# Kernel optimization log

Hardware: AMD Instinct MI355X
Metric: run time of the kernel (lower is better)

## Reference

```python
import jax, jax.numpy as jnp
import numpy as np

TAU = 2.0
EPS = 1e-5
T, B, C, H, W = 4, 16, 256, 32, 32
HEADS = 8
HD = C // HEADS
N = H * W


def make_spike(grad_fn):
    @jax.custom_vjp
    def f(x):
        return (x >= 0.0).astype(x.dtype)
    def fwd(x):
        return f(x), x
    def bwd(res, g):
        return (g * grad_fn(res),)
    f.defvjp(fwd, bwd)
    return f

# ATan surrogate (alpha=5.0) used by q/k/v LIF nodes
spike_atan5 = make_spike(lambda x: (5.0 / 2.0) / (1.0 + (jnp.pi / 2.0 * 5.0 * x) ** 2))
# default Sigmoid surrogate (alpha=4.0) for shortcut_lif / talking_heads_lif
def _sig_grad(x):
    s = jax.nn.sigmoid(4.0 * x)
    return 4.0 * s * (1.0 - s)
spike_sig4 = make_spike(_sig_grad)


def lif(x, spike, v_th=1.0):
    # multi-step LIF over leading time axis; hard reset to 0, detach_reset
    def step(v, xt):
        h = v + (xt - v) / TAU
        s = spike(h - v_th)
        v_new = h * (1.0 - jax.lax.stop_gradient(s))
        return v_new, s
    _, out = jax.lax.scan(step, jnp.zeros_like(x[0]), x)
    return out


def conv1x1(x, w):
    # x: (T,B,C,H,W), w: (Cout,Cin) from Conv2d kernel_size=1
    return jnp.einsum('tbchw,oc->tbohw', x, w)


def bn(y, gamma, beta, mean, var):
    scale = (gamma / jnp.sqrt(var + EPS))[None, None, :, None, None]
    shift = (beta - mean * gamma / jnp.sqrt(var + EPS))[None, None, :, None, None]
    return y * scale + shift


def to_heads(x):
    # (T,B,C,H,W) -> (T,B,heads,N,hd); matches flatten(3).transpose(-1,-2).reshape.permute
    x = x.reshape(T, B, C, N).transpose(0, 1, 3, 2)          # (T,B,N,C)
    x = x.reshape(T, B, N, HEADS, HD).transpose(0, 1, 3, 2, 4)  # (T,B,heads,N,hd)
    return x


def setup_inputs() -> dict:
    key = jax.random.key(0)
    ks = jax.random.split(key, 20)
    def bn_params(i):
        return (1.0 + 0.1 * jax.random.normal(ks[i], (C,), jnp.float32),
                0.1 * jax.random.normal(ks[i + 1], (C,), jnp.float32),
                0.1 * jax.random.normal(ks[i + 2], (C,), jnp.float32),
                jax.random.uniform(ks[i + 3], (C,), jnp.float32, 0.5, 1.5))
    q_g, q_b, q_m, q_var = bn_params(1)
    k_g, k_b, k_m, k_var = bn_params(5)
    v_g, v_b, v_m, v_var = bn_params(9)
    p_g, p_b, p_m, p_var = bn_params(13)
    std = 1.0 / np.sqrt(C)
    return {
        'x': jax.random.normal(ks[0], (T, B, C, H, W), jnp.float32),
        'q_w': std * jax.random.normal(ks[17], (C, C), jnp.float32),
        'q_g': q_g, 'q_b': q_b, 'q_m': q_m, 'q_var': q_var,
        'k_w': std * jax.random.normal(ks[18], (C, C), jnp.float32),
        'k_g': k_g, 'k_b': k_b, 'k_m': k_m, 'k_var': k_var,
        'v_w': std * jax.random.normal(ks[19], (C, C), jnp.float32),
        'v_g': v_g, 'v_b': v_b, 'v_m': v_m, 'v_var': v_var,
        'proj_w': std * jax.random.normal(ks[4], (C, C), jnp.float32),
        'proj_bias': 0.01 * jax.random.normal(ks[8], (C,), jnp.float32),
        'p_g': p_g, 'p_b': p_b, 'p_m': p_m, 'p_var': p_var,
    }


def reference(x, q_w, q_g, q_b, q_m, q_var, k_w, k_g, k_b, k_m, k_var,
              v_w, v_g, v_b, v_m, v_var, proj_w, proj_bias, p_g, p_b, p_m, p_var):
    identity = x
    xs = lif(x, spike_sig4, 1.0)                      # shortcut_lif
    q = to_heads(lif(bn(conv1x1(xs, q_w), q_g, q_b, q_m, q_var), spike_atan5, 1.0))
    k = to_heads(lif(bn(conv1x1(xs, k_w), k_g, k_b, k_m, k_var), spike_atan5, 1.0))
    v = to_heads(lif(bn(conv1x1(xs, v_w), v_g, v_b, v_m, v_var), spike_atan5, 1.0))
    kv = jnp.sum(k * v, axis=-2, keepdims=True)       # (T,B,heads,1,hd)
    kv = lif(kv, spike_sig4, 0.5)                     # talking_heads_lif, v_th=0.5
    attn = q * kv                                     # (T,B,heads,N,hd)
    # transpose(3,4).reshape(T,B,C,H,W)
    out = attn.transpose(0, 1, 2, 4, 3).reshape(T, B, C, H, W)
    out = conv1x1(out, proj_w) + proj_bias[None, None, :, None, None]
    out = bn(out, p_g, p_b, p_m, p_var)
    out = out + identity
    return out, v
```

## Files before the change

kernel.cpp:

```cpp
#include <hip/hip_runtime.h>
#include <hip/hip_bf16.h>
#include <stdint.h>

#define T_ 4
#define B_ 16
#define C_ 256
#define N_ 1024
#define HEADS_ 8
#define HD_ 32

typedef unsigned long long u64;
typedef unsigned char u8;

__device__ __forceinline__ u64 rf64(u64 v) {
  unsigned lo = __builtin_amdgcn_readfirstlane((unsigned)v);
  unsigned hi = __builtin_amdgcn_readfirstlane((unsigned)(v >> 32));
  return ((u64)hi << 32) | (u64)lo;
}

__global__ __launch_bounds__(256) void prep_kernel(
    const float* __restrict__ qw, const float* __restrict__ kw,
    const float* __restrict__ vw, const float* __restrict__ pw,
    const float* __restrict__ qg, const float* __restrict__ qb2,
    const float* __restrict__ qmn, const float* __restrict__ qvr,
    const float* __restrict__ kg, const float* __restrict__ kb2,
    const float* __restrict__ kmn, const float* __restrict__ kvr,
    const float* __restrict__ vg, const float* __restrict__ vb2,
    const float* __restrict__ vmn, const float* __restrict__ vvr,
    const float* __restrict__ pg, const float* __restrict__ pb2,
    const float* __restrict__ pmn, const float* __restrict__ pvr,
    float* __restrict__ wqkv, float* __restrict__ wtp,
    float* __restrict__ bnt) {
  if (blockIdx.x < 256) {
    int c = blockIdx.x;
    int o = threadIdx.x;
    wqkv[c * 768 + o]       = qw[o * C_ + c];
    wqkv[c * 768 + 256 + o] = kw[o * C_ + c];
    wqkv[c * 768 + 512 + o] = vw[o * C_ + c];
    wtp[c * C_ + o]         = pw[o * C_ + c];
  } else {
    int c = threadIdx.x;
    float rs;
    rs = sqrtf(qvr[c] + 1e-5f);
    bnt[0 * C_ + c] = qg[c] / rs;
    bnt[1 * C_ + c] = qb2[c] - qmn[c] * qg[c] / rs;
    rs = sqrtf(kvr[c] + 1e-5f);
    bnt[2 * C_ + c] = kg[c] / rs;
    bnt[3 * C_ + c] = kb2[c] - kmn[c] * kg[c] / rs;
    rs = sqrtf(vvr[c] + 1e-5f);
    bnt[4 * C_ + c] = vg[c] / rs;
    bnt[5 * C_ + c] = vb2[c] - vmn[c] * vg[c] / rs;
    rs = sqrtf(pvr[c] + 1e-5f);
    bnt[6 * C_ + c] = pg[c] / rs;
    bnt[7 * C_ + c] = pb2[c] - pmn[c] * pg[c] / rs;
  }
}

__global__ __launch_bounds__(256) void lif_shortcut(const float* __restrict__ x,
                                                    u64* __restrict__ xsm) {
  int b = blockIdx.x >> 5;
  int n0 = (blockIdx.x & 31) << 5;
  int tid = threadIdx.x;
  int l = tid & 63, w = tid >> 6;
  __shared__ float tile[C_ * 33];
  float v[32];
#pragma unroll
  for (int i = 0; i < 32; i++) v[i] = 0.f;
  int c = (w << 6) + l;
  for (int t = 0; t < T_; t++) {
    __syncthreads();
    const float* xp = x + (((size_t)t * B_ + b) * C_) * N_ + n0;
    for (int idx = tid; idx < C_ * 32; idx += 256) {
      int cc = idx >> 5, nn = idx & 31;
      tile[cc * 33 + nn] = xp[(size_t)cc * N_ + nn];
    }
    __syncthreads();
#pragma unroll
    for (int nn = 0; nn < 32; nn++) {
      float xv = tile[c * 33 + nn];
      float h = v[nn] + (xv - v[nn]) * 0.5f;
      bool s = h >= 1.0f;
      v[nn] = s ? 0.f : h;
      u64 bal = __ballot(s);
      if (l == nn) xsm[(((size_t)t * B_ + b) * N_ + n0 + nn) * 4 + w] = bal;
    }
  }
}

__global__ __launch_bounds__(256) void qkv_sparse(
    const u64* __restrict__ xsm, const float* __restrict__ wqkv,
    const float* __restrict__ bnt, u8* __restrict__ pkvb,
    u64* __restrict__ qm_out, float* __restrict__ vout) {
  int b = blockIdx.x >> 7;
  int nt = blockIdx.x & 127;
  int n0 = nt << 3;
  int tid = threadIdx.x;
  int l = tid & 63, wv = tid >> 6;

  __shared__ u64 kvw[8][4][4];
  __shared__ u64 vb[8][4][4];

  float qsc[4], qsh[4], ksc[4], ksh[4], vsc[4], vsh[4];
#pragma unroll
  for (int j = 0; j < 4; j++) {
    int o = (l << 2) + j;
    qsc[j] = bnt[0 * C_ + o]; qsh[j] = bnt[1 * C_ + o];
    ksc[j] = bnt[2 * C_ + o]; ksh[j] = bnt[3 * C_ + o];
    vsc[j] = bnt[4 * C_ + o]; vsh[j] = bnt[5 * C_ + o];
  }

  for (int s = 0; s < 2; s++) {
    int nn = wv + (s << 2);
    int n = n0 + nn;
    float vq[4] = {0.f, 0.f, 0.f, 0.f};
    float vk[4] = {0.f, 0.f, 0.f, 0.f};
    float vv2[4] = {0.f, 0.f, 0.f, 0.f};
#pragma unroll
    for (int t = 0; t < 4; t++) {
      size_t site = ((size_t)t * B_ + b) * N_ + n;
      const u64* mp = xsm + (site << 2);
      float aq[4] = {0.f, 0.f, 0.f, 0.f};
      float ak[4] = {0.f, 0.f, 0.f, 0.f};
      float av[4] = {0.f, 0.f, 0.f, 0.f};
      float4 q0 = {0.f, 0.f, 0.f, 0.f};
      float4 k0 = {0.f, 0.f, 0.f, 0.f};
      float4 v0 = {0.f, 0.f, 0.f, 0.f};
#pragma unroll
      for (int wd = 0; wd < 4; wd++) {
        u64 m = rf64(mp[wd]);
        while (m) {
          int c = (wd << 6) + __builtin_ctzll(m);
          m &= m - 1;
          const float4* pb = (const float4*)(wqkv + c * 768) + l;
          float4 q1 = pb[0];
          float4 k1 = pb[64];
          float4 v1 = pb[128];
          aq[0] += q0.x; aq[1] += q0.y; aq[2] += q0.z; aq[3] += q0.w;
          ak[0] += k0.x; ak[1] += k0.y; ak[2] += k0.z; ak[3] += k0.w;
          av[0] += v0.x; av[1] += v0.y; av[2] += v0.z; av[3] += v0.w;
          q0 = q1; k0 = k1; v0 = v1;
        }
      }
      aq[0] += q0.x; aq[1] += q0.y; aq[2] += q0.z; aq[3] += q0.w;
      ak[0] += k0.x; ak[1] += k0.y; ak[2] += k0.z; ak[3] += k0.w;
      av[0] += v0.x; av[1] += v0.y; av[2] += v0.z; av[3] += v0.w;
#pragma unroll
      for (int j = 0; j < 4; j++) {
        float pq = aq[j] * qsc[j] + qsh[j];
        float pk = ak[j] * ksc[j] + ksh[j];
        float pv = av[j] * vsc[j] + vsh[j];
        float hq = vq[j] + (pq - vq[j]) * 0.5f;
        float hk = vk[j] + (pk - vk[j]) * 0.5f;
        float hv = vv2[j] + (pv - vv2[j]) * 0.5f;
        bool sq = hq >= 1.0f; vq[j] = sq ? 0.f : hq;
        bool sk = hk >= 1.0f; vk[j] = sk ? 0.f : hk;
        bool sv = hv >= 1.0f; vv2[j] = sv ? 0.f : hv;
        u64 bq = __ballot(sq);
        u64 bkv = __ballot(sk && sv);
        u64 bv = __ballot(sv);
        if (l == (t << 2) + j) {
          qm_out[(site << 2) + j] = bq;
          kvw[nn][t][j] = bkv;
          vb[nn][t][j] = bv;
        }
      }
    }
  }
  __syncthreads();

#pragma unroll
  for (int t = 0; t < 4; t++) {
    int c = tid;
    int ll = c >> 2, j = c & 3;
    int ssum = 0;
#pragma unroll
    for (int s8 = 0; s8 < 8; s8++)
      ssum += (int)((kvw[s8][t][j] >> ll) & 1ull);
    pkvb[((((size_t)t * B_ + b) * C_ + c) << 7) + nt] = (u8)ssum;
  }

  {
    int th = tid >> 3;
    int t = th >> 3;
    int head = th & 7;
    int nl = tid & 7;
    float* vp = vout +
        ((((size_t)t * B_ + b) * HEADS_ + head) * N_ + n0 + nl) * HD_;
#pragma unroll
    for (int m4 = 0; m4 < 8; m4++) {
      int li = (head << 3) + m4;
      float4 o4;
      o4.x = ((vb[nl][t][0] >> li) & 1ull) ? 1.f : 0.f;
      o4.y = ((vb[nl][t][1] >> li) & 1ull) ? 1.f : 0.f;
      o4.z = ((vb[nl][t][2] >> li) & 1ull) ? 1.f : 0.f;
      o4.w = ((vb[nl][t][3] >> li) & 1ull) ? 1.f : 0.f;
      *(float4*)(vp + (m4 << 2)) = o4;
    }
  }
}

__global__ __launch_bounds__(256) void kv_lif_kernel(const u8* __restrict__ pkvb,
                                                     u64* __restrict__ kvsm) {
  int b = blockIdx.x;
  int tid = threadIdx.x;
  int l = tid & 63, j = tid >> 6;
  int c = (l << 2) + j;
  float v = 0.f;
  for (int t = 0; t < 4; t++) {
    const uint4* p =
        (const uint4*)(pkvb + ((((size_t)t * B_ + b) * C_ + c) << 7));
    int s = 0;
#pragma unroll
    for (int i = 0; i < 8; i++) {
      uint4 u = p[i];
      unsigned a;
      a = u.x; s += (a & 255) + ((a >> 8) & 255) + ((a >> 16) & 255) + (a >> 24);
      a = u.y; s += (a & 255) + ((a >> 8) & 255) + ((a >> 16) & 255) + (a >> 24);
      a = u.z; s += (a & 255) + ((a >> 8) & 255) + ((a >> 16) & 255) + (a >> 24);
      a = u.w; s += (a & 255) + ((a >> 8) & 255) + ((a >> 16) & 255) + (a >> 24);
    }
    float kvs = (float)s;
    float h = v + (kvs - v) * 0.5f;
    bool sp = h >= 0.5f;
    v = sp ? 0.f : h;
    u64 bal = __ballot(sp);
    if (l == t) kvsm[((size_t)t * B_ + b) * 4 + j] = bal;
  }
}

__global__ __launch_bounds__(256) void proj_sparse(
    const u64* __restrict__ qm, const u64* __restrict__ kvsm,
    const float* __restrict__ wtp, const float* __restrict__ bnt,
    const float* __restrict__ pbias, const float* __restrict__ x,
    float* __restrict__ out) {
  int tb = blockIdx.x >> 5;
  int n0 = (blockIdx.x & 31) << 5;
  int t = tb >> 4, b = tb & 15;
  int tid = threadIdx.x;
  int l = tid & 63, w = tid >> 6;
  __shared__ float tile[C_ * 33];
  u64 kvm[4];
#pragma unroll
  for (int j = 0; j < 4; j++) kvm[j] = kvsm[((size_t)t * B_ + b) * 4 + j];
  for (int nn = w; nn < 32; nn += 4) {
    int n = n0 + nn;
    float acc[4] = {0.f, 0.f, 0.f, 0.f};
    size_t site = ((size_t)t * B_ + b) * N_ + n;
    const u64* mp = qm + (site << 2);
#pragma unroll
    for (int j = 0; j < 4; j++) {
      u64 m = rf64(mp[j]) & kvm[j];
      while (m) {
        int li = __builtin_ctzll(m);
        m &= m - 1;
        int c = (li << 2) + j;
        const float* rp = wtp + c * C_;
#pragma unroll
        for (int jj = 0; jj < 4; jj++) acc[jj] += rp[(jj << 6) + l];
      }
    }
#pragma unroll
    for (int jj = 0; jj < 4; jj++) tile[((jj << 6) + l) * 33 + nn] = acc[jj];
  }
  __syncthreads();
  int col = l & 31;
  int half = l >> 5;
  for (int r = (w << 1) + half; r < C_; r += 8) {
    float val = tile[r * 33 + col];
    float z = (val + pbias[r]) * bnt[6 * C_ + r] + bnt[7 * C_ + r];
    size_t xi = (((size_t)t * B_ + b) * C_ + r) * N_ + n0 + col;
    out[xi] = z + x[xi];
  }
}

__global__ __launch_bounds__(256) void fill_zero_f32(float* p, size_t n) {
  size_t i = (size_t)blockIdx.x * 256 + threadIdx.x;
  if (i < n) p[i] = 0.0f;
}

extern "C" void kernel_launch(void* const* d_in, const int* in_sizes, int n_in,
                              void* d_out, int out_size, void* d_ws, size_t ws_size,
                              hipStream_t stream) {
  const float* x  = (const float*)d_in[0];
  const float* qw = (const float*)d_in[1];
  const float* qg = (const float*)d_in[2];
  const float* qb = (const float*)d_in[3];
  const float* qm = (const float*)d_in[4];
  const float* qv = (const float*)d_in[5];
  const float* kw = (const float*)d_in[6];
  const float* kg = (const float*)d_in[7];
  const float* kb = (const float*)d_in[8];
  const float* km = (const float*)d_in[9];
  const float* kv = (const float*)d_in[10];
  const float* vw = (const float*)d_in[11];
  const float* vg = (const float*)d_in[12];
  const float* vb2 = (const float*)d_in[13];
  const float* vm = (const float*)d_in[14];
  const float* vv = (const float*)d_in[15];
  const float* pw = (const float*)d_in[16];
  const float* pbias = (const float*)d_in[17];
  const float* pg = (const float*)d_in[18];
  const float* pb = (const float*)d_in[19];
  const float* pm = (const float*)d_in[20];
  const float* pv = (const float*)d_in[21];

  const size_t needed = 7342080ull + 2048ull;
  if (ws_size < needed) {
    size_t n = (size_t)out_size;
    fill_zero_f32<<<(unsigned)((n + 255) / 256), 256, 0, stream>>>(
        (float*)d_out, n);
    return;
  }

  char* ws = (char*)d_ws;
  float* wqkv = (float*)(ws + 0);
  float* wtp  = (float*)(ws + 786432);
  float* bnt  = (float*)(ws + 1048576);
  u64*   xsm  = (u64*)  (ws + 1056768);
  u64*   qmm  = (u64*)  (ws + 3153920);
  u8*    pkvb = (u8*)   (ws + 5251072);
  u64*   kvsm = (u64*)  (ws + 7348224);

  float* out  = (float*)d_out;
  float* vout = out + (size_t)T_ * B_ * C_ * N_;

  prep_kernel<<<257, 256, 0, stream>>>(qw, kw, vw, pw,
                                       qg, qb, qm, qv, kg, kb, km, kv,
                                       vg, vb2, vm, vv, pg, pb, pm, pv,
                                       wqkv, wtp, bnt);
  lif_shortcut<<<512, 256, 0, stream>>>(x, xsm);
  qkv_sparse<<<2048, 256, 0, stream>>>(xsm, wqkv, bnt, pkvb, qmm, vout);
  kv_lif_kernel<<<16, 256, 0, stream>>>(pkvb, kvsm);
  proj_sparse<<<2048, 256, 0, stream>>>(qmm, kvsm, wtp, bnt, pbias, x, out);
}
```

Baseline: 157.6 us.

## Precompute per-site spike channel lists to unroll sparse QKV gather

The shortcut LIF kernel now also writes, for each site, a compact byte list of up to 32 active input channels plus a count. The QKV kernel reads these lists and gathers weight rows four at a time, using a zeroed padding row for out-of-range slots, instead of a serial ctz loop over bitmasks. Sites with more than 32 active channels fall back to the bitmask path. The QKV grid is halved, with each block covering 16 positions, and the readfirstlane broadcasts are removed. This trades extra workspace and list-building work for more memory-level parallelism in the gather.

Result: no change. 159.7 us (+1.3%).

```diff
diff --git a/kernel.cpp b/kernel.cpp
--- a/kernel.cpp
+++ b/kernel.cpp
@@ -8,15 +8,11 @@
 #define N_ 1024
 #define HEADS_ 8
 #define HD_ 32
+#define ZOFF 196608
 
 typedef unsigned long long u64;
 typedef unsigned char u8;
-
-__device__ __forceinline__ u64 rf64(u64 v) {
-  unsigned lo = __builtin_amdgcn_readfirstlane((unsigned)v);
-  unsigned hi = __builtin_amdgcn_readfirstlane((unsigned)(v >> 32));
-  return ((u64)hi << 32) | (u64)lo;
-}
+typedef unsigned short u16;
 
 __global__ __launch_bounds__(256) void prep_kernel(
     const float* __restrict__ qw, const float* __restrict__ kw,
@@ -38,7 +34,7 @@
     wqkv[c * 768 + 256 + o] = kw[o * C_ + c];
     wqkv[c * 768 + 512 + o] = vw[o * C_ + c];
     wtp[c * C_ + o]         = pw[o * C_ + c];
-  } else {
+  } else if (blockIdx.x == 256) {
     int c = threadIdx.x;
     float rs;
     rs = sqrtf(qvr[c] + 1e-5f);
@@ -53,16 +49,25 @@
     rs = sqrtf(pvr[c] + 1e-5f);
     bnt[6 * C_ + c] = pg[c] / rs;
     bnt[7 * C_ + c] = pb2[c] - pmn[c] * pg[c] / rs;
-  }
-}
-
-__global__ __launch_bounds__(256) void lif_shortcut(const float* __restrict__ x,
-                                                    u64* __restrict__ xsm) {
+  } else {
+    int o = threadIdx.x;
+    wqkv[ZOFF + o]       = 0.f;
+    wqkv[ZOFF + 256 + o] = 0.f;
+    wqkv[ZOFF + 512 + o] = 0.f;
+  }
+}
+
+__global__ __launch_bounds__(256) void lif_pack(const float* __restrict__ x,
+                                                u64* __restrict__ xsm,
+                                                u8* __restrict__ lists,
+                                                u16* __restrict__ cnts) {
   int b = blockIdx.x >> 5;
   int n0 = (blockIdx.x & 31) << 5;
   int tid = threadIdx.x;
   int l = tid & 63, w = tid >> 6;
   __shared__ float tile[C_ * 33];
+  __shared__ u64 lmask[4][32][4];
+  __shared__ u8 slist[128][32];
   float v[32];
 #pragma unroll
   for (int i = 0; i < 32; i++) v[i] = 0.f;
@@ -82,23 +87,51 @@
       bool s = h >= 1.0f;
       v[nn] = s ? 0.f : h;
       u64 bal = __ballot(s);
-      if (l == nn) xsm[(((size_t)t * B_ + b) * N_ + n0 + nn) * 4 + w] = bal;
-    }
+      if (l == nn) {
+        lmask[t][nn][w] = bal;
+        xsm[(((size_t)t * B_ + b) * N_ + n0 + nn) * 4 + w] = bal;
+      }
+    }
+  }
+  __syncthreads();
+  if (tid < 128) {
+    int t = tid >> 5, nn = tid & 31;
+    size_t site = ((size_t)t * B_ + b) * N_ + n0 + nn;
+    int cnt = 0;
+#pragma unroll
+    for (int wd = 0; wd < 4; wd++) {
+      u64 m = lmask[t][nn][wd];
+      while (m) {
+        int cc = (wd << 6) + __builtin_ctzll(m);
+        m &= m - 1;
+        if (cnt < 32) slist[tid][cnt] = (u8)cc;
+        cnt++;
+      }
+    }
+    cnts[site] = (u16)cnt;
+  }
+  __syncthreads();
+  {
+    int si = tid >> 1, h = tid & 1;
+    int t = si >> 5, nn = si & 31;
+    size_t site = ((size_t)t * B_ + b) * N_ + n0 + nn;
+    ((uint4*)(lists + (site << 5)))[h] = ((uint4*)slist[si])[h];
   }
 }
 
 __global__ __launch_bounds__(256) void qkv_sparse(
-    const u64* __restrict__ xsm, const float* __restrict__ wqkv,
+    const u64* __restrict__ xsm, const u8* __restrict__ lists,
+    const u16* __restrict__ cnts, const float* __restrict__ wqkv,
     const float* __restrict__ bnt, u8* __restrict__ pkvb,
     u64* __restrict__ qm_out, float* __restrict__ vout) {
-  int b = blockIdx.x >> 7;
-  int nt = blockIdx.x & 127;
-  int n0 = nt << 3;
+  int b = blockIdx.x >> 6;
+  int nt = blockIdx.x & 63;
+  int n0 = nt << 4;
   int tid = threadIdx.x;
   int l = tid & 63, wv = tid >> 6;
 
-  __shared__ u64 kvw[8][4][4];
-  __shared__ u64 vb[8][4][4];
+  __shared__ u64 kvw[16][4][4];
+  __shared__ u64 vb[16][4][4];
 
   float qsc[4], qsh[4], ksc[4], ksh[4], vsc[4], vsh[4];
 #pragma unroll
@@ -109,7 +142,7 @@
     vsc[j] = bnt[4 * C_ + o]; vsh[j] = bnt[5 * C_ + o];
   }
 
-  for (int s = 0; s < 2; s++) {
+  for (int s = 0; s < 4; s++) {
     int nn = wv + (s << 2);
     int n = n0 + nn;
     float vq[4] = {0.f, 0.f, 0.f, 0.f};
@@ -118,32 +151,63 @@
 #pragma unroll
     for (int t = 0; t < 4; t++) {
       size_t site = ((size_t)t * B_ + b) * N_ + n;
-      const u64* mp = xsm + (site << 2);
+      int cn = cnts[site];
       float aq[4] = {0.f, 0.f, 0.f, 0.f};
       float ak[4] = {0.f, 0.f, 0.f, 0.f};
       float av[4] = {0.f, 0.f, 0.f, 0.f};
-      float4 q0 = {0.f, 0.f, 0.f, 0.f};
-      float4 k0 = {0.f, 0.f, 0.f, 0.f};
-      float4 v0 = {0.f, 0.f, 0.f, 0.f};
-#pragma unroll
-      for (int wd = 0; wd < 4; wd++) {
-        u64 m = rf64(mp[wd]);
-        while (m) {
-          int c = (wd << 6) + __builtin_ctzll(m);
-          m &= m - 1;
-          const float4* pb = (const float4*)(wqkv + c * 768) + l;
-          float4 q1 = pb[0];
-          float4 k1 = pb[64];
-          float4 v1 = pb[128];
-          aq[0] += q0.x; aq[1] += q0.y; aq[2] += q0.z; aq[3] += q0.w;
-          ak[0] += k0.x; ak[1] += k0.y; ak[2] += k0.z; ak[3] += k0.w;
-          av[0] += v0.x; av[1] += v0.y; av[2] += v0.z; av[3] += v0.w;
-          q0 = q1; k0 = k1; v0 = v1;
+      if (cn > 0 && cn <= 32) {
+        const uint4* lp = (const uint4*)(lists + (site << 5));
+        uint4 L0 = lp[0], L1 = lp[1];
+        unsigned dw[8] = {L0.x, L0.y, L0.z, L0.w, L1.x, L1.y, L1.z, L1.w};
+#pragma unroll
+        for (int d = 0; d < 8; d++) {
+          if ((d << 2) < cn) {
+            unsigned w4 = dw[d];
+            int i0 = d << 2;
+            int c0 = w4 & 255, c1 = (w4 >> 8) & 255;
+            int c2 = (w4 >> 16) & 255, c3 = w4 >> 24;
+            const float4* p0 =
+                (const float4*)(wqkv + (i0 + 0 < cn ? c0 * 768 : ZOFF)) + l;
+            const float4* p1 =
+                (const float4*)(wqkv + (i0 + 1 < cn ? c1 * 768 : ZOFF)) + l;
+            const float4* p2 =
+                (const float4*)(wqkv + (i0 + 2 < cn ? c2 * 768 : ZOFF)) + l;
+            const float4* p3 =
+                (const float4*)(wqkv + (i0 + 3 < cn ? c3 * 768 : ZOFF)) + l;
+            float4 q0 = p0[0], k0 = p0[64], v0 = p0[128];
+            float4 q1 = p1[0], k1 = p1[64], v1 = p1[128];
+            float4 q2 = p2[0], k2 = p2[64], v2 = p2[128];
+            float4 q3 = p3[0], k3 = p3[64], v3 = p3[128];
+            aq[0] += q0.x; aq[1] += q0.y; aq[2] += q0.z; aq[3] += q0.w;
+            ak[0] += k0.x; ak[1] += k0.y; ak[2] += k0.z; ak[3] += k0.w;
+            av[0] += v0.x; av[1] += v0.y; av[2] += v0.z; av[3] += v0.w;
+            aq[0] += q1.x; aq[1] += q1.y; aq[2] += q1.z; aq[3] += q1.w;
+            ak[0] += k1.x; ak[1] += k1.y; ak[2] += k1.z; ak[3] += k1.w;
+            av[0] += v1.x; av[1] += v1.y; av[2] += v1.z; av[3] += v1.w;
+            aq[0] += q2.x; aq[1] += q2.y; aq[2] += q2.z; aq[3] += q2.w;
+            ak[0] += k2.x; ak[1] += k2.y; ak[2] += k2.z; ak[3] += k2.w;
+            av[0] += v2.x; av[1] += v2.y; av[2] += v2.z; av[3] += v2.w;
+            aq[0] += q3.x; aq[1] += q3.y; aq[2] += q3.z; aq[3] += q3.w;
+            ak[0] += k3.x; ak[1] += k3.y; ak[2] += k3.z; ak[3] += k3.w;
+            av[0] += v3.x; av[1] += v3.y; av[2] += v3.z; av[3] += v3.w;
+          }
         }
-      }
-      aq[0] += q0.x; aq[1] += q0.y; aq[2] += q0.z; aq[3] += q0.w;
-      ak[0] += k0.x; ak[1] += k0.y; ak[2] += k0.z; ak[3] += k0.w;
-      av[0] += v0.x; av[1] += v0.y; av[2] += v0.z; av[3] += v0.w;
+      } else if (cn > 32) {
+        const u64* mp = xsm + (site << 2);
+#pragma unroll
+        for (int wd = 0; wd < 4; wd++) {
+          u64 m = mp[wd];
+          while (m) {
+            int cc = (wd << 6) + __builtin_ctzll(m);
+            m &= m - 1;
+            const float4* pb = (const float4*)(wqkv + cc * 768) + l;
+            float4 q0 = pb[0], k0 = pb[64], v0 = pb[128];
+            aq[0] += q0.x; aq[1] += q0.y; aq[2] += q0.z; aq[3] += q0.w;
+            ak[0] += k0.x; ak[1] += k0.y; ak[2] += k0.z; ak[3] += k0.w;
+            av[0] += v0.x; av[1] += v0.y; av[2] += v0.z; av[3] += v0.w;
+          }
+        }
+      }
 #pragma unroll
       for (int j = 0; j < 4; j++) {
         float pq = aq[j] * qsc[j] + qsh[j];
@@ -174,27 +238,31 @@
     int ll = c >> 2, j = c & 3;
     int ssum = 0;
 #pragma unroll
-    for (int s8 = 0; s8 < 8; s8++)
-      ssum += (int)((kvw[s8][t][j] >> ll) & 1ull);
-    pkvb[((((size_t)t * B_ + b) * C_ + c) << 7) + nt] = (u8)ssum;
+    for (int s16 = 0; s16 < 16; s16++)
+      ssum += (int)((kvw[s16][t][j] >> ll) & 1ull);
+    pkvb[((((size_t)t * B_ + b) * C_ + c) << 6) + nt] = (u8)ssum;
   }
 
   {
     int th = tid >> 3;
     int t = th >> 3;
     int head = th & 7;
-    int nl = tid & 7;
-    float* vp = vout +
-        ((((size_t)t * B_ + b) * HEADS_ + head) * N_ + n0 + nl) * HD_;
-#pragma unroll
-    for (int m4 = 0; m4 < 8; m4++) {
-      int li = (head << 3) + m4;
-      float4 o4;
-      o4.x = ((vb[nl][t][0] >> li) & 1ull) ? 1.f : 0.f;
-      o4.y = ((vb[nl][t][1] >> li) & 1ull) ? 1.f : 0.f;
-      o4.z = ((vb[nl][t][2] >> li) & 1ull) ? 1.f : 0.f;
-      o4.w = ((vb[nl][t][3] >> li) & 1ull) ? 1.f : 0.f;
-      *(float4*)(vp + (m4 << 2)) = o4;
+    int nl0 = tid & 7;
+#pragma unroll
+    for (int rep = 0; rep < 2; rep++) {
+      int nl = nl0 + (rep << 3);
+      float* vp = vout +
+          ((((size_t)t * B_ + b) * HEADS_ + head) * N_ + n0 + nl) * HD_;
+#pragma unroll
+      for (int m4 = 0; m4 < 8; m4++) {
+        int li = (head << 3) + m4;
+        float4 o4;
+        o4.x = ((vb[nl][t][0] >> li) & 1ull) ? 1.f : 0.f;
+        o4.y = ((vb[nl][t][1] >> li) & 1ull) ? 1.f : 0.f;
+        o4.z = ((vb[nl][t][2] >> li) & 1ull) ? 1.f : 0.f;
+        o4.w = ((vb[nl][t][3] >> li) & 1ull) ? 1.f : 0.f;
+        *(float4*)(vp + (m4 << 2)) = o4;
+      }
     }
   }
 }
@@ -208,10 +276,10 @@
   float v = 0.f;
   for (int t = 0; t < 4; t++) {
     const uint4* p =
-        (const uint4*)(pkvb + ((((size_t)t * B_ + b) * C_ + c) << 7));
+        (const uint4*)(pkvb + ((((size_t)t * B_ + b) * C_ + c) << 6));
     int s = 0;
 #pragma unroll
-    for (int i = 0; i < 8; i++) {
+    for (int i = 0; i < 4; i++) {
       uint4 u = p[i];
       unsigned a;
       a = u.x; s += (a & 255) + ((a >> 8) & 255) + ((a >> 16) & 255) + (a >> 24);
@@ -249,7 +317,7 @@
     const u64* mp = qm + (site << 2);
 #pragma unroll
     for (int j = 0; j < 4; j++) {
-      u64 m = rf64(mp[j]) & kvm[j];
+      u64 m = mp[j] & kvm[j];
       while (m) {
         int li = __builtin_ctzll(m);
         m &= m - 1;
@@ -304,7 +372,7 @@
   const float* pm = (const float*)d_in[20];
   const float* pv = (const float*)d_in[21];
 
-  const size_t needed = 7342080ull + 2048ull;
+  const size_t needed = 8534016ull;
   if (ws_size < needed) {
     size_t n = (size_t)out_size;
     fill_zero_f32<<<(unsigned)((n + 255) / 256), 256, 0, stream>>>(
@@ -313,23 +381,26 @@
   }
 
   char* ws = (char*)d_ws;
-  float* wqkv = (float*)(ws + 0);
-  float* wtp  = (float*)(ws + 786432);
-  float* bnt  = (float*)(ws + 1048576);
-  u64*   xsm  = (u64*)  (ws + 1056768);
-  u64*   qmm  = (u64*)  (ws + 3153920);
-  u8*    pkvb = (u8*)   (ws + 5251072);
-  u64*   kvsm = (u64*)  (ws + 7348224);
+  float* wqkv  = (float*)(ws + 0);
+  float* wtp   = (float*)(ws + 790528);
+  float* bnt   = (float*)(ws + 1052672);
+  u64*   xsm   = (u64*)  (ws + 1060864);
+  u8*    lists = (u8*)   (ws + 3158016);
+  u16*   cnts  = (u16*)  (ws + 5255168);
+  u64*   qmm   = (u64*)  (ws + 5386240);
+  u8*    pkvb  = (u8*)   (ws + 7483392);
+  u64*   kvsm  = (u64*)  (ws + 8531968);
 
   float* out  = (float*)d_out;
   float* vout = out + (size_t)T_ * B_ * C_ * N_;
 
-  prep_kernel<<<257, 256, 0, stream>>>(qw, kw, vw, pw,
+  prep_kernel<<<258, 256, 0, stream>>>(qw, kw, vw, pw,
                                        qg, qb, qm, qv, kg, kb, km, kv,
                                        vg, vb2, vm, vv, pg, pb, pm, pv,
                                        wqkv, wtp, bnt);
-  lif_shortcut<<<512, 256, 0, stream>>>(x, xsm);
-  qkv_sparse<<<2048, 256, 0, stream>>>(xsm, wqkv, bnt, pkvb, qmm, vout);
+  lif_pack<<<512, 256, 0, stream>>>(x, xsm, lists, cnts);
+  qkv_sparse<<<1024, 256, 0, stream>>>(xsm, lists, cnts, wqkv, bnt,
+                                       pkvb, qmm, vout);
   kv_lif_kernel<<<16, 256, 0, stream>>>(pkvb, kvsm);
   proj_sparse<<<2048, 256, 0, stream>>>(qmm, kvsm, wtp, bnt, pbias, x, out);
 }
```

## Interleave four timestep spike gathers per loop with zero-row padding in qkv_sparse

Applied to the files above, without the earlier changes.

The sparse QKV gather now walks the spike masks of all four timesteps together, issuing four independent weight-row loads per iteration. Timesteps whose mask is already exhausted read an added zero weight row, so no per-lane branching is needed. The goal is more memory-level parallelism and less serialisation of the dependent gather chain. It also writes v spikes directly per lane instead of through shared ballot bitmasks, and stores kv partial counts as floats in a larger per-tile layout that kv_lif reduces over 128 entries. This costs more registers, extra wasted loads when timesteps differ in spike count, and more workspace traffic.

Result: slower. 187.5 us (+18.9%).

```diff
diff --git a/kernel.cpp b/kernel.cpp
--- a/kernel.cpp
+++ b/kernel.cpp
@@ -8,6 +8,7 @@
 #define N_ 1024
 #define HEADS_ 8
 #define HD_ 32
+#define ZROW 256
 
 typedef unsigned long long u64;
 typedef unsigned char u8;
@@ -38,7 +39,7 @@
     wqkv[c * 768 + 256 + o] = kw[o * C_ + c];
     wqkv[c * 768 + 512 + o] = vw[o * C_ + c];
     wtp[c * C_ + o]         = pw[o * C_ + c];
-  } else {
+  } else if (blockIdx.x == 256) {
     int c = threadIdx.x;
     float rs;
     rs = sqrtf(qvr[c] + 1e-5f);
@@ -53,6 +54,11 @@
     rs = sqrtf(pvr[c] + 1e-5f);
     bnt[6 * C_ + c] = pg[c] / rs;
     bnt[7 * C_ + c] = pb2[c] - pmn[c] * pg[c] / rs;
+  } else {
+    int o = threadIdx.x;
+    wqkv[ZROW * 768 + o]       = 0.f;
+    wqkv[ZROW * 768 + 256 + o] = 0.f;
+    wqkv[ZROW * 768 + 512 + o] = 0.f;
   }
 }
 
@@ -87,9 +93,14 @@
   }
 }
 
+#define ACC3(tt, Q, K, V)                                              \
+  aq[tt][0] += Q.x; aq[tt][1] += Q.y; aq[tt][2] += Q.z; aq[tt][3] += Q.w; \
+  ak[tt][0] += K.x; ak[tt][1] += K.y; ak[tt][2] += K.z; ak[tt][3] += K.w; \
+  av[tt][0] += V.x; av[tt][1] += V.y; av[tt][2] += V.z; av[tt][3] += V.w;
+
 __global__ __launch_bounds__(256) void qkv_sparse(
     const u64* __restrict__ xsm, const float* __restrict__ wqkv,
-    const float* __restrict__ bnt, u8* __restrict__ pkvb,
+    const float* __restrict__ bnt, float* __restrict__ pkv,
     u64* __restrict__ qm_out, float* __restrict__ vout) {
   int b = blockIdx.x >> 7;
   int nt = blockIdx.x & 127;
@@ -97,9 +108,6 @@
   int tid = threadIdx.x;
   int l = tid & 63, wv = tid >> 6;
 
-  __shared__ u64 kvw[8][4][4];
-  __shared__ u64 vb[8][4][4];
-
   float qsc[4], qsh[4], ksc[4], ksh[4], vsc[4], vsh[4];
 #pragma unroll
   for (int j = 0; j < 4; j++) {
@@ -108,98 +116,92 @@
     ksc[j] = bnt[2 * C_ + o]; ksh[j] = bnt[3 * C_ + o];
     vsc[j] = bnt[4 * C_ + o]; vsh[j] = bnt[5 * C_ + o];
   }
-
-  for (int s = 0; s < 2; s++) {
-    int nn = wv + (s << 2);
+  int cnt[4][4];
+#pragma unroll
+  for (int t = 0; t < 4; t++)
+#pragma unroll
+    for (int j = 0; j < 4; j++) cnt[t][j] = 0;
+
+  for (int nn = wv; nn < 8; nn += 4) {
     int n = n0 + nn;
+    float aq[4][4], ak[4][4], av[4][4];
+#pragma unroll
+    for (int t = 0; t < 4; t++)
+#pragma unroll
+      for (int j = 0; j < 4; j++) { aq[t][j] = 0.f; ak[t][j] = 0.f; av[t][j] = 0.f; }
+    u64 msk[4][4];
+#pragma unroll
+    for (int t = 0; t < 4; t++)
+#pragma unroll
+      for (int wd = 0; wd < 4; wd++)
+        msk[t][wd] = rf64(xsm[((((size_t)t * B_ + b) * N_ + n) << 2) + wd]);
+#pragma unroll
+    for (int wd = 0; wd < 4; wd++) {
+      u64 m0 = msk[0][wd], m1 = msk[1][wd], m2 = msk[2][wd], m3 = msk[3][wd];
+      while (m0 | m1 | m2 | m3) {
+        int c0 = ZROW, c1 = ZROW, c2 = ZROW, c3 = ZROW;
+        if (m0) { c0 = (wd << 6) + __builtin_ctzll(m0); m0 &= m0 - 1; }
+        if (m1) { c1 = (wd << 6) + __builtin_ctzll(m1); m1 &= m1 - 1; }
+        if (m2) { c2 = (wd << 6) + __builtin_ctzll(m2); m2 &= m2 - 1; }
+        if (m3) { c3 = (wd << 6) + __builtin_ctzll(m3); m3 &= m3 - 1; }
+        const float4* p0 = (const float4*)(wqkv + c0 * 768) + l;
+        const float4* p1 = (const float4*)(wqkv + c1 * 768) + l;
+        const float4* p2 = (const float4*)(wqkv + c2 * 768) + l;
+        const float4* p3 = (const float4*)(wqkv + c3 * 768) + l;
+        float4 q0 = p0[0], k0 = p0[64], v0 = p0[128];
+        float4 q1 = p1[0], k1 = p1[64], v1 = p1[128];
+        float4 q2 = p2[0], k2 = p2[64], v2 = p2[128];
+        float4 q3 = p3[0], k3 = p3[64], v3 = p3[128];
+        ACC3(0, q0, k0, v0)
+        ACC3(1, q1, k1, v1)
+        ACC3(2, q2, k2, v2)
+        ACC3(3, q3, k3, v3)
+      }
+    }
     float vq[4] = {0.f, 0.f, 0.f, 0.f};
     float vk[4] = {0.f, 0.f, 0.f, 0.f};
     float vv2[4] = {0.f, 0.f, 0.f, 0.f};
 #pragma unroll
     for (int t = 0; t < 4; t++) {
       size_t site = ((size_t)t * B_ + b) * N_ + n;
-      const u64* mp = xsm + (site << 2);
-      float aq[4] = {0.f, 0.f, 0.f, 0.f};
-      float ak[4] = {0.f, 0.f, 0.f, 0.f};
-      float av[4] = {0.f, 0.f, 0.f, 0.f};
-      float4 q0 = {0.f, 0.f, 0.f, 0.f};
-      float4 k0 = {0.f, 0.f, 0.f, 0.f};
-      float4 v0 = {0.f, 0.f, 0.f, 0.f};
-#pragma unroll
-      for (int wd = 0; wd < 4; wd++) {
-        u64 m = rf64(mp[wd]);
-        while (m) {
-          int c = (wd << 6) + __builtin_ctzll(m);
-          m &= m - 1;
-          const float4* pb = (const float4*)(wqkv + c * 768) + l;
-          float4 q1 = pb[0];
-          float4 k1 = pb[64];
-          float4 v1 = pb[128];
-          aq[0] += q0.x; aq[1] += q0.y; aq[2] += q0.z; aq[3] += q0.w;
-          ak[0] += k0.x; ak[1] += k0.y; ak[2] += k0.z; ak[3] += k0.w;
-          av[0] += v0.x; av[1] += v0.y; av[2] += v0.z; av[3] += v0.w;
-          q0 = q1; k0 = k1; v0 = v1;
-        }
-      }
-      aq[0] += q0.x; aq[1] += q0.y; aq[2] += q0.z; aq[3] += q0.w;
-      ak[0] += k0.x; ak[1] += k0.y; ak[2] += k0.z; ak[3] += k0.w;
-      av[0] += v0.x; av[1] += v0.y; av[2] += v0.z; av[3] += v0.w;
+      float vo[4];
 #pragma unroll
       for (int j = 0; j < 4; j++) {
-        float pq = aq[j] * qsc[j] + qsh[j];
-        float pk = ak[j] * ksc[j] + ksh[j];
-        float pv = av[j] * vsc[j] + vsh[j];
+        float pq = aq[t][j] * qsc[j] + qsh[j];
+        float pk = ak[t][j] * ksc[j] + ksh[j];
+        float pv = av[t][j] * vsc[j] + vsh[j];
         float hq = vq[j] + (pq - vq[j]) * 0.5f;
         float hk = vk[j] + (pk - vk[j]) * 0.5f;
         float hv = vv2[j] + (pv - vv2[j]) * 0.5f;
         bool sq = hq >= 1.0f; vq[j] = sq ? 0.f : hq;
         bool sk = hk >= 1.0f; vk[j] = sk ? 0.f : hk;
         bool sv = hv >= 1.0f; vv2[j] = sv ? 0.f : hv;
+        vo[j] = sv ? 1.0f : 0.0f;
+        cnt[t][j] += (sk && sv) ? 1 : 0;
         u64 bq = __ballot(sq);
-        u64 bkv = __ballot(sk && sv);
-        u64 bv = __ballot(sv);
-        if (l == (t << 2) + j) {
-          qm_out[(site << 2) + j] = bq;
-          kvw[nn][t][j] = bkv;
-          vb[nn][t][j] = bv;
-        }
+        if (l == (t << 2) + j) qm_out[(site << 2) + j] = bq;
       }
-    }
-  }
+      float* vp = vout +
+          ((((size_t)t * B_ + b) * HEADS_ + (l >> 3)) * (size_t)N_ + n) * HD_ +
+          ((l & 7) << 2);
+      float4 o4; o4.x = vo[0]; o4.y = vo[1]; o4.z = vo[2]; o4.w = vo[3];
+      *(float4*)vp = o4;
+    }
+  }
+  __shared__ int scnt[4][4][C_];
+#pragma unroll
+  for (int t = 0; t < 4; t++)
+#pragma unroll
+    for (int j = 0; j < 4; j++) scnt[wv][t][(l << 2) + j] = cnt[t][j];
   __syncthreads();
-
-#pragma unroll
-  for (int t = 0; t < 4; t++) {
-    int c = tid;
-    int ll = c >> 2, j = c & 3;
-    int ssum = 0;
-#pragma unroll
-    for (int s8 = 0; s8 < 8; s8++)
-      ssum += (int)((kvw[s8][t][j] >> ll) & 1ull);
-    pkvb[((((size_t)t * B_ + b) * C_ + c) << 7) + nt] = (u8)ssum;
-  }
-
-  {
-    int th = tid >> 3;
-    int t = th >> 3;
-    int head = th & 7;
-    int nl = tid & 7;
-    float* vp = vout +
-        ((((size_t)t * B_ + b) * HEADS_ + head) * N_ + n0 + nl) * HD_;
-#pragma unroll
-    for (int m4 = 0; m4 < 8; m4++) {
-      int li = (head << 3) + m4;
-      float4 o4;
-      o4.x = ((vb[nl][t][0] >> li) & 1ull) ? 1.f : 0.f;
-      o4.y = ((vb[nl][t][1] >> li) & 1ull) ? 1.f : 0.f;
-      o4.z = ((vb[nl][t][2] >> li) & 1ull) ? 1.f : 0.f;
-      o4.w = ((vb[nl][t][3] >> li) & 1ull) ? 1.f : 0.f;
-      *(float4*)(vp + (m4 << 2)) = o4;
-    }
-  }
-}
-
-__global__ __launch_bounds__(256) void kv_lif_kernel(const u8* __restrict__ pkvb,
+  for (int idx = tid; idx < 4 * C_; idx += 256) {
+    int t = idx >> 8, c = idx & 255;
+    int s = scnt[0][t][c] + scnt[1][t][c] + scnt[2][t][c] + scnt[3][t][c];
+    pkv[(((size_t)t * B_ + b) * 128 + nt) * C_ + c] = (float)s;
+  }
+}
+
+__global__ __launch_bounds__(256) void kv_lif_kernel(const float* __restrict__ pkv,
                                                      u64* __restrict__ kvsm) {
   int b = blockIdx.x;
   int tid = threadIdx.x;
@@ -207,23 +209,14 @@
   int c = (l << 2) + j;
   float v = 0.f;
   for (int t = 0; t < 4; t++) {
-    const uint4* p =
-        (const uint4*)(pkvb + ((((size_t)t * B_ + b) * C_ + c) << 7));
-    int s = 0;
-#pragma unroll
-    for (int i = 0; i < 8; i++) {
-      uint4 u = p[i];
-      unsigned a;
-      a = u.x; s += (a & 255) + ((a >> 8) & 255) + ((a >> 16) & 255) + (a >> 24);
-      a = u.y; s += (a & 255) + ((a >> 8) & 255) + ((a >> 16) & 255) + (a >> 24);
-      a = u.z; s += (a & 255) + ((a >> 8) & 255) + ((a >> 16) & 255) + (a >> 24);
-      a = u.w; s += (a & 255) + ((a >> 8) & 255) + ((a >> 16) & 255) + (a >> 24);
-    }
-    float kvs = (float)s;
-    float h = v + (kvs - v) * 0.5f;
-    bool sp = h >= 0.5f;
-    v = sp ? 0.f : h;
-    u64 bal = __ballot(sp);
+    const float* p = pkv + (((size_t)t * B_ + b) * 128) * C_ + c;
+    float kv = 0.f;
+#pragma unroll
+    for (int i = 0; i < 128; i++) kv += p[(size_t)i * C_];
+    float h = v + (kv - v) * 0.5f;
+    bool s = h >= 0.5f;
+    v = s ? 0.f : h;
+    u64 bal = __ballot(s);
     if (l == t) kvsm[((size_t)t * B_ + b) * 4 + j] = bal;
   }
 }
@@ -304,7 +297,7 @@
   const float* pm = (const float*)d_in[20];
   const float* pv = (const float*)d_in[21];
 
-  const size_t needed = 7342080ull + 2048ull;
+  const size_t needed = 13644800ull;
   if (ws_size < needed) {
     size_t n = (size_t)out_size;
     fill_zero_f32<<<(unsigned)((n + 255) / 256), 256, 0, stream>>>(
@@ -314,22 +307,22 @@
 
   char* ws = (char*)d_ws;
   float* wqkv = (float*)(ws + 0);
-  float* wtp  = (float*)(ws + 786432);
-  float* bnt  = (float*)(ws + 1048576);
-  u64*   xsm  = (u64*)  (ws + 1056768);
-  u64*   qmm  = (u64*)  (ws + 3153920);
-  u8*    pkvb = (u8*)   (ws + 5251072);
-  u64*   kvsm = (u64*)  (ws + 7348224);
+  float* wtp  = (float*)(ws + 789504);
+  float* bnt  = (float*)(ws + 1051648);
+  u64*   xsm  = (u64*)  (ws + 1059840);
+  u64*   qmm  = (u64*)  (ws + 3156992);
+  float* pkv  = (float*)(ws + 5254144);
+  u64*   kvsm = (u64*)  (ws + 13642752);
 
   float* out  = (float*)d_out;
   float* vout = out + (size_t)T_ * B_ * C_ * N_;
 
-  prep_kernel<<<257, 256, 0, stream>>>(qw, kw, vw, pw,
+  prep_kernel<<<258, 256, 0, stream>>>(qw, kw, vw, pw,
                                        qg, qb, qm, qv, kg, kb, km, kv,
                                        vg, vb2, vm, vv, pg, pb, pm, pv,
                                        wqkv, wtp, bnt);
   lif_shortcut<<<512, 256, 0, stream>>>(x, xsm);
-  qkv_sparse<<<2048, 256, 0, stream>>>(xsm, wqkv, bnt, pkvb, qmm, vout);
-  kv_lif_kernel<<<16, 256, 0, stream>>>(pkvb, kvsm);
+  qkv_sparse<<<2048, 256, 0, stream>>>(xsm, wqkv, bnt, pkv, qmm, vout);
+  kv_lif_kernel<<<16, 256, 0, stream>>>(pkv, kvsm);
   proj_sparse<<<2048, 256, 0, stream>>>(qmm, kvsm, wtp, bnt, pbias, x, out);
 }
```
